# Optimization experiments

Measured on AMD Instinct MI355X. Metric: run time of the kernel, lower is better.

The kernel has to match this reference:

```python
import jax, jax.numpy as jnp
import numpy as np

EPS = 1e-5
N_GRAPHS = 64


def gcn_conv(x, W, b, src, dst, n_nodes):
    # GCNConv: out = D^{-1/2} (A + I) D^{-1/2} X W + b
    xw = x @ W  # [N, H]
    # add self loops
    loops = jnp.arange(n_nodes, dtype=src.dtype)
    src_f = jnp.concatenate([src, loops])
    dst_f = jnp.concatenate([dst, loops])
    deg = jax.ops.segment_sum(jnp.ones_like(dst_f, dtype=xw.dtype), dst_f, num_segments=n_nodes)
    dinv = jnp.where(deg > 0, jax.lax.rsqrt(deg), 0.0)
    norm = dinv[src_f] * dinv[dst_f]  # [E+N]
    msg = xw[src_f] * norm[:, None]  # gather + scale
    out = jax.ops.segment_sum(msg, dst_f, num_segments=n_nodes)  # scatter-add
    return out + b


def batchnorm(x):
    # fresh BatchNorm1d in training mode: identity affine, batch stats, biased var
    mean = jnp.mean(x, axis=0)
    var = jnp.mean((x - mean) ** 2, axis=0)
    return (x - mean) * jax.lax.rsqrt(var + EPS)


def setup_inputs() -> dict:
    key = jax.random.key(0)
    ks = jax.random.split(key, 12)
    N, E, F, H, C = 65536, 1048576, 64, 64, 16
    x = jax.random.normal(ks[0], (N, F), dtype=jnp.float32)
    edge_index = jax.random.randint(ks[1], (2, E), 0, N, dtype=jnp.int64)
    batch = jnp.sort(jax.random.randint(ks[2], (N,), 0, N_GRAPHS, dtype=jnp.int64))
    s = 1.0 / np.sqrt(H)
    W0 = jax.random.normal(ks[3], (F, H), dtype=jnp.float32) * s
    b0 = jax.random.normal(ks[4], (H,), dtype=jnp.float32) * 0.1
    W1 = jax.random.normal(ks[5], (H, H), dtype=jnp.float32) * s
    b1 = jax.random.normal(ks[6], (H,), dtype=jnp.float32) * 0.1
    W2 = jax.random.normal(ks[7], (H, H), dtype=jnp.float32) * s
    b2 = jax.random.normal(ks[8], (H,), dtype=jnp.float32) * 0.1
    clf_W = jax.random.normal(ks[9], (C, H), dtype=jnp.float32) * s
    clf_b = jax.random.normal(ks[10], (C,), dtype=jnp.float32) * 0.1
    return {"x": x, "edge_index": edge_index, "batch": batch,
            "W0": W0, "b0": b0, "W1": W1, "b1": b1, "W2": W2, "b2": b2,
            "clf_W": clf_W, "clf_b": clf_b}


def reference(x, edge_index, batch, W0, b0, W1, b1, W2, b2, clf_W, clf_b):
    n_nodes = x.shape[0]
    src, dst = edge_index[0], edge_index[1]
    weights = [(W0, b0), (W1, b1), (W2, b2)]
    n_conv = len(weights)
    h = x
    for i, (W, b) in enumerate(weights):
        h = gcn_conv(h, W, b, src, dst, n_nodes)
        if i < n_conv - 1:
            h = jax.nn.relu(h)
        h = batchnorm(h)
    # global mean pool over graphs
    sums = jax.ops.segment_sum(h, batch, num_segments=N_GRAPHS)
    cnts = jax.ops.segment_sum(jnp.ones((n_nodes,), h.dtype), batch, num_segments=N_GRAPHS)
    pooled = sums / jnp.maximum(cnts, 1.0)[:, None]
    logits = pooled @ clf_W.T + clf_b
    return jax.nn.softmax(logits, axis=1)
```

## Files before the change

### kernel.cpp

```cpp
#include <hip/hip_runtime.h>
#include <hip/hip_fp16.h>


#define NBKT 512
#define CAP  4096
#define BSTRIDE 16

__device__ inline unsigned pack2h(float a, float b) {
    __half ha = __float2half_rn(a), hb = __float2half_rn(b);
    unsigned short ua = *(unsigned short*)&ha, ub = *(unsigned short*)&hb;
    return (unsigned)ua | ((unsigned)ub << 16);
}

__device__ inline void acc8(float* a, uint4 u) {
    __half2* hp = (__half2*)&u;
#pragma unroll
    for (int i = 0; i < 4; ++i) {
        float2 f = __half22float2(hp[i]);
        a[2 * i] += f.x;
        a[2 * i + 1] += f.y;
    }
}

__global__ void k_binit(int* __restrict__ bcur) {
    int t = blockIdx.x * 256 + threadIdx.x;
    if (t < NBKT) bcur[t * BSTRIDE] = t * CAP;
}

__global__ void k_bin(const int* __restrict__ ei, int E, int* __restrict__ bcur,
                      int* __restrict__ buck) {
    __shared__ int sd[4096];
    __shared__ unsigned short bk[4096];
    __shared__ int cnt[NBKT], off[NBKT];
    int t = threadIdx.x;
    int base = blockIdx.x * 4096;
    for (int i = t; i < NBKT; i += 256) cnt[i] = 0;
    __syncthreads();
#pragma unroll
    for (int k = 0; k < 16; ++k) {
        int i = k * 256 + t;
        int e = base + i;
        int s = ei[e], d = ei[E + e];
        sd[i] = (s << 7) | (d & 127);
        int b = d >> 7;
        bk[i] = (unsigned short)b;
        atomicAdd(&cnt[b], 1);
    }
    __syncthreads();
    for (int b = t; b < NBKT; b += 256) {
        int c = cnt[b];
        off[b] = c ? atomicAdd(&bcur[b * BSTRIDE], c) : 0;
    }
    __syncthreads();
#pragma unroll
    for (int k = 0; k < 16; ++k) {
        int i = k * 256 + t;
        int b = bk[i];
        int p = atomicAdd(&off[b], 1);
        buck[p] = sd[i];
    }
}

__global__ void k_scanB(const int* __restrict__ bcur, int* __restrict__ bbase,
                        int* __restrict__ rowptr, float* __restrict__ psum,
                        float* __restrict__ pcnt, int N, int E) {
    __shared__ int s[NBKT];
    int t = threadIdx.x;
    int v = bcur[t * BSTRIDE] - t * CAP;
    s[t] = v;
    __syncthreads();
    for (int o = 1; o < NBKT; o <<= 1) {
        int x = (t >= o) ? s[t - o] : 0;
        __syncthreads();
        s[t] += x;
        __syncthreads();
    }
    bbase[t] = s[t] - v;
    for (int i = t; i < 4096; i += NBKT) psum[i] = 0.0f;
    if (t < 64) pcnt[t] = 0.0f;
    if (t == 0) rowptr[N] = E;
}

__global__ void k_place(const int* __restrict__ bcur, const int* __restrict__ buck,
                        const int* __restrict__ bbase, int* __restrict__ rowptr,
                        float* __restrict__ dinv, int* __restrict__ csr) {
    __shared__ int dc[128], sc[128], cur[128];
    int b = blockIdx.x, t = threadIdx.x;
    if (t < 128) dc[t] = 0;
    __syncthreads();
    int beg = b * CAP, end = bcur[b * BSTRIDE];
    for (int i = beg + t; i < end; i += 256) atomicAdd(&dc[buck[i] & 127], 1);
    __syncthreads();
    int v = (t < 128) ? dc[t] : 0;
    if (t < 128) sc[t] = v;
    __syncthreads();
    for (int o = 1; o < 128; o <<= 1) {
        int x = 0;
        if (t < 128 && t >= o) x = sc[t - o];
        __syncthreads();
        if (t < 128) sc[t] += x;
        __syncthreads();
    }
    if (t < 128) {
        int r = bbase[b] + sc[t] - v;
        rowptr[b * 128 + t] = r;
        cur[t] = r;
        dinv[b * 128 + t] = rsqrtf((float)(v + 1));
    }
    __syncthreads();
    for (int i = beg + t; i < end; i += 256) {
        int e = buck[i];
        int p = atomicAdd(&cur[e & 127], 1);
        csr[p] = e >> 7;
    }
}

template <int HIN>
__global__ void k_gemm(const void* __restrict__ hv, const float* __restrict__ W,
                       const float* __restrict__ mean, const float* __restrict__ rstd,
                       int has_stats, const float* __restrict__ dinv,
                       __half* __restrict__ y) {
    __shared__ float Ws[4096];
    __shared__ float hs[64 * 65];
    __shared__ float sm[64], sr[64], bs[64];
    int t = threadIdx.x;
    int rowBase = blockIdx.x * 64;
    if (t < 64) {
        sm[t] = has_stats ? mean[t] : 0.0f;
        sr[t] = has_stats ? rstd[t] : 1.0f;
    }
    __syncthreads();
#pragma unroll
    for (int k = 0; k < 4; ++k) {
        int i = t + k * 256;
        float4 wv = ((const float4*)W)[i];
        float s = sr[i >> 4];
        wv.x *= s; wv.y *= s; wv.z *= s; wv.w *= s;
        ((float4*)Ws)[i] = wv;
    }
    if (HIN) {
        const uint4* src = (const uint4*)((const __half*)hv + (size_t)rowBase * 64);
#pragma unroll
        for (int k = 0; k < 2; ++k) {
            int i = t + k * 256;
            int row = i >> 3, c8 = i & 7;
            uint4 u = src[i];
            const __half2* hp = (const __half2*)&u;
            float* dst = &hs[row * 65 + c8 * 8];
#pragma unroll
            for (int j = 0; j < 4; ++j) {
                dst[2 * j + 0] = __low2float(hp[j]);
                dst[2 * j + 1] = __high2float(hp[j]);
            }
        }
    } else {
        const float4* src = (const float4*)((const float*)hv + (size_t)rowBase * 64);
#pragma unroll
        for (int k = 0; k < 4; ++k) {
            int i = t + k * 256;
            int row = i >> 4, c4 = i & 15;
            float4 v = src[i];
            float* dst = &hs[row * 65 + c4 * 4];
            dst[0] = v.x; dst[1] = v.y; dst[2] = v.z; dst[3] = v.w;
        }
    }
    __syncthreads();
    if (t < 64) {
        float acc = 0.0f;
        for (int f = 0; f < 64; ++f) acc += sm[f] * Ws[f * 64 + t];
        bs[t] = -acc;
    }
    __syncthreads();
    int rg = t >> 4;
    int cg = t & 15;
    float4 a0, a1, a2, a3;
    {
        float bx = bs[cg * 4 + 0], by = bs[cg * 4 + 1];
        float bz = bs[cg * 4 + 2], bw = bs[cg * 4 + 3];
        a0 = {bx, by, bz, bw}; a1 = a0; a2 = a0; a3 = a0;
    }
    const float* h0 = &hs[(rg * 4 + 0) * 65];
    const float* h1 = &hs[(rg * 4 + 1) * 65];
    const float* h2 = &hs[(rg * 4 + 2) * 65];
    const float* h3 = &hs[(rg * 4 + 3) * 65];
#pragma unroll 4
    for (int f = 0; f < 64; ++f) {
        float4 wv = ((float4*)Ws)[f * 16 + cg];
        float v0 = h0[f], v1 = h1[f], v2 = h2[f], v3 = h3[f];
        a0.x += v0 * wv.x; a0.y += v0 * wv.y; a0.z += v0 * wv.z; a0.w += v0 * wv.w;
        a1.x += v1 * wv.x; a1.y += v1 * wv.y; a1.z += v1 * wv.z; a1.w += v1 * wv.w;
        a2.x += v2 * wv.x; a2.y += v2 * wv.y; a2.z += v2 * wv.z; a2.w += v2 * wv.w;
        a3.x += v3 * wv.x; a3.y += v3 * wv.y; a3.z += v3 * wv.z; a3.w += v3 * wv.w;
    }
    float d0 = dinv[rowBase + rg * 4 + 0];
    float d1 = dinv[rowBase + rg * 4 + 1];
    float d2 = dinv[rowBase + rg * 4 + 2];
    float d3 = dinv[rowBase + rg * 4 + 3];
    uint2* y2 = (uint2*)y;
    size_t ob = (size_t)(rowBase + rg * 4) * 16 + cg;
    y2[ob + 0]  = {pack2h(a0.x * d0, a0.y * d0), pack2h(a0.z * d0, a0.w * d0)};
    y2[ob + 16] = {pack2h(a1.x * d1, a1.y * d1), pack2h(a1.z * d1, a1.w * d1)};
    y2[ob + 32] = {pack2h(a2.x * d2, a2.y * d2), pack2h(a2.z * d2, a2.w * d2)};
    y2[ob + 48] = {pack2h(a3.x * d3, a3.y * d3), pack2h(a3.z * d3, a3.w * d3)};
}

template <int RELU>
__global__ __launch_bounds__(512) void k_agg(
        const __half* __restrict__ y, const int* __restrict__ rowptr,
        const int* __restrict__ csr, const float* __restrict__ dinv,
        const float* __restrict__ bias, __half* __restrict__ hout,
        float* __restrict__ partials, int N) {
    __shared__ int lcsr[2048];
    __shared__ int lrp[65];
    __shared__ float SW[16][64];
    int t = threadIdx.x;
    int lane = t & 63, wid = t >> 6;
    int o = lane >> 3, j = lane & 7;
    int nodeBase = blockIdx.x * 64;
    if (t < 65) lrp[t] = rowptr[nodeBase + t];
    __syncthreads();
    int wbase = lrp[0];
    int wlen = lrp[64] - wbase;
    bool fits = (wlen <= 2048);
    if (fits)
        for (int i = t; i < wlen; i += 512) lcsr[i] = csr[wbase + i];
    __syncthreads();

    int n = nodeBase + wid * 8 + o;
    int beg = lrp[wid * 8 + o] - wbase;
    int d = lrp[wid * 8 + o + 1] - wbase - beg;
    const uint4* y4 = (const uint4*)y;
    float a[8] = {0, 0, 0, 0, 0, 0, 0, 0};

    if (fits) {
        const int* cp = lcsr + beg;
        int k = 0;
        for (; k + 4 <= d; k += 4) {
            int s0 = cp[k], s1 = cp[k + 1], s2 = cp[k + 2], s3 = cp[k + 3];
            uint4 u0 = y4[(size_t)s0 * 8 + j];
            uint4 u1 = y4[(size_t)s1 * 8 + j];
            uint4 u2 = y4[(size_t)s2 * 8 + j];
            uint4 u3 = y4[(size_t)s3 * 8 + j];
            acc8(a, u0); acc8(a, u1); acc8(a, u2); acc8(a, u3);
        }
        for (; k < d; ++k) {
            uint4 u0 = y4[(size_t)cp[k] * 8 + j];
            acc8(a, u0);
        }
    } else {
        const int* cp = csr + wbase + beg;
        int k = 0;
        for (; k + 4 <= d; k += 4) {
            int s0 = cp[k], s1 = cp[k + 1], s2 = cp[k + 2], s3 = cp[k + 3];
            uint4 u0 = y4[(size_t)s0 * 8 + j];
            uint4 u1 = y4[(size_t)s1 * 8 + j];
            uint4 u2 = y4[(size_t)s2 * 8 + j];
            uint4 u3 = y4[(size_t)s3 * 8 + j];
            acc8(a, u0); acc8(a, u1); acc8(a, u2); acc8(a, u3);
        }
        for (; k < d; ++k) {
            uint4 u0 = y4[(size_t)cp[k] * 8 + j];
            acc8(a, u0);
        }
    }
    uint4 us = y4[(size_t)n * 8 + j];
    acc8(a, us);

    float dv = dinv[n];
    const float4* b4 = (const float4*)bias;
    float4 blo = b4[j * 2], bhi = b4[j * 2 + 1];
    float v[8];
    v[0] = a[0] * dv + blo.x; v[1] = a[1] * dv + blo.y;
    v[2] = a[2] * dv + blo.z; v[3] = a[3] * dv + blo.w;
    v[4] = a[4] * dv + bhi.x; v[5] = a[5] * dv + bhi.y;
    v[6] = a[6] * dv + bhi.z; v[7] = a[7] * dv + bhi.w;
    if (RELU) {
#pragma unroll
        for (int i = 0; i < 8; ++i) v[i] = fmaxf(v[i], 0.0f);
    }
    uint4 ov;
    ov.x = pack2h(v[0], v[1]); ov.y = pack2h(v[2], v[3]);
    ov.z = pack2h(v[4], v[5]); ov.w = pack2h(v[6], v[7]);
    ((uint4*)hout)[(size_t)n * 8 + j] = ov;

    float q[8];
#pragma unroll
    for (int i = 0; i < 8; ++i) q[i] = v[i] * v[i];
#pragma unroll
    for (int st = 8; st <= 32; st <<= 1) {
#pragma unroll
        for (int i = 0; i < 8; ++i) {
            v[i] += __shfl_xor(v[i], st);
            q[i] += __shfl_xor(q[i], st);
        }
    }
    if (o == 0) {
#pragma unroll
        for (int i = 0; i < 8; ++i) {
            SW[wid][j * 8 + i] = v[i];
            SW[8 + wid][j * 8 + i] = q[i];
        }
    }
    __syncthreads();
    if (t < 64) {
        float s = 0.0f, qq = 0.0f;
#pragma unroll
        for (int w = 0; w < 8; ++w) {
            s += SW[w][t];
            qq += SW[8 + w][t];
        }
        partials[(size_t)blockIdx.x * 128 + t] = s;
        partials[(size_t)blockIdx.x * 128 + 64 + t] = qq;
    }
}

__global__ void k_stats(const float* __restrict__ partials, int nblk,
                        float* __restrict__ mean, float* __restrict__ rstd, float invN) {
    __shared__ float sh[256];
    int f = blockIdx.x, t = threadIdx.x;
    float s = 0.0f, q = 0.0f;
    for (int b = t; b < nblk; b += 256) {
        s += partials[(size_t)b * 128 + f];
        q += partials[(size_t)b * 128 + 64 + f];
    }
    sh[t] = s;
    __syncthreads();
    for (int o = 128; o > 0; o >>= 1) {
        if (t < o) sh[t] += sh[t + o];
        __syncthreads();
    }
    float S = sh[0];
    __syncthreads();
    sh[t] = q;
    __syncthreads();
    for (int o = 128; o > 0; o >>= 1) {
        if (t < o) sh[t] += sh[t + o];
        __syncthreads();
    }
    if (t == 0) {
        float Qs = sh[0];
        float m = S * invN;
        float var = Qs * invN - m * m;
        mean[f] = m;
        rstd[f] = rsqrtf(var + 1e-5f);
    }
}

__global__ void k_pool(const __half* __restrict__ h, const int* __restrict__ batch,
                       const float* __restrict__ mean, const float* __restrict__ rstd,
                       float* __restrict__ psum, float* __restrict__ pcnt) {
    int lane = threadIdx.x;
    int base = blockIdx.x * 64;
    float m = mean[lane], r = rstd[lane];
    int cur = batch[base];
    float acc = 0.0f;
    int runlen = 0;
    for (int i = 0; i < 64; ++i) {
        int n = base + i;
        int g = batch[n];
        if (g != cur) {
            atomicAdd(&psum[cur * 64 + lane], acc);
            if (lane == 0) atomicAdd(&pcnt[cur], (float)runlen);
            acc = 0.0f;
            runlen = 0;
            cur = g;
        }
        acc += (__half2float(h[(size_t)n * 64 + lane]) - m) * r;
        runlen++;
    }
    atomicAdd(&psum[cur * 64 + lane], acc);
    if (lane == 0) atomicAdd(&pcnt[cur], (float)runlen);
}

__global__ void k_head(const float* __restrict__ psum, const float* __restrict__ pcnt,
                       const float* __restrict__ clfW, const float* __restrict__ clfb,
                       float* __restrict__ out) {
    __shared__ float ps[64 * 64];
    __shared__ float wl[16 * 64];
    __shared__ float ci[64];
    int t = threadIdx.x;
    ((float4*)ps)[t] = ((const float4*)psum)[t];
    if (t < 256) ((float4*)wl)[t] = ((const float4*)clfW)[t];
    if (t < 64) ci[t] = 1.0f / fmaxf(pcnt[t], 1.0f);
    __syncthreads();
    int g = t >> 4, c = t & 15;
    float acc = 0.0f;
#pragma unroll 8
    for (int f = 0; f < 64; ++f) acc += ps[g * 64 + f] * wl[c * 64 + f];
    acc = acc * ci[g] + clfb[c];
    float mx = acc;
    for (int o = 1; o < 16; o <<= 1) mx = fmaxf(mx, __shfl_xor(mx, o, 16));
    float e = __expf(acc - mx);
    float s = e;
    for (int o = 1; o < 16; o <<= 1) s += __shfl_xor(s, o, 16);
    out[t] = e / s;
}

extern "C" void kernel_launch(void* const* d_in, const int* in_sizes, int n_in,
                              void* d_out, int out_size, void* d_ws, size_t ws_size,
                              hipStream_t stream) {
    const float* x    = (const float*)d_in[0];
    const int*   ei   = (const int*)d_in[1];
    const int*   bat  = (const int*)d_in[2];
    const float* W0   = (const float*)d_in[3];
    const float* b0   = (const float*)d_in[4];
    const float* W1   = (const float*)d_in[5];
    const float* b1   = (const float*)d_in[6];
    const float* W2   = (const float*)d_in[7];
    const float* b2   = (const float*)d_in[8];
    const float* clfW = (const float*)d_in[9];
    const float* clfb = (const float*)d_in[10];
    float* out = (float*)d_out;

    const int N = in_sizes[0] / 64;
    const int E = in_sizes[1] / 2;
    const int AB = N / 64;

    char* w = (char*)d_ws;
    size_t off = 0;
    auto take = [&](size_t bytes) -> void* {
        off = (off + 255) & ~(size_t)255;
        void* p = w + off;
        off += bytes;
        return p;
    };
    int*    rowptr   = (int*)take((size_t)(N + 1) * 4);
    int*    bcur     = (int*)take((size_t)NBKT * BSTRIDE * 4);
    int*    bbase    = (int*)take((size_t)NBKT * 4);
    float*  dinv     = (float*)take((size_t)N * 4);
    int*    csr      = (int*)take((size_t)E * 4);
    __half* y        = (__half*)take((size_t)N * 64 * 2);
    __half* hA       = (__half*)take((size_t)N * 64 * 2);
    __half* hB       = (__half*)take((size_t)N * 64 * 2);
    float*  partials = (float*)take((size_t)AB * 128 * 4);
    float*  mean     = (float*)take(256);
    float*  rstd     = (float*)take(256);
    float*  psum     = (float*)take(64 * 64 * 4);
    float*  pcnt     = (float*)take(64 * 4);
    int* buck = (int*)hB;

    k_binit<<<(NBKT + 255) / 256, 256, 0, stream>>>(bcur);
    k_bin<<<E / 4096, 256, 0, stream>>>(ei, E, bcur, buck);
    k_scanB<<<1, NBKT, 0, stream>>>(bcur, bbase, rowptr, psum, pcnt, N, E);
    k_place<<<NBKT, 256, 0, stream>>>(bcur, buck, bbase, rowptr, dinv, csr);

    const float invN = 1.0f / (float)N;

    k_gemm<0><<<N / 64, 256, 0, stream>>>(x, W0, mean, rstd, 0, dinv, y);
    k_agg<1><<<AB, 512, 0, stream>>>(y, rowptr, csr, dinv, b0, hA, partials, N);
    k_stats<<<64, 256, 0, stream>>>(partials, AB, mean, rstd, invN);

    k_gemm<1><<<N / 64, 256, 0, stream>>>(hA, W1, mean, rstd, 1, dinv, y);
    k_agg<1><<<AB, 512, 0, stream>>>(y, rowptr, csr, dinv, b1, hB, partials, N);
    k_stats<<<64, 256, 0, stream>>>(partials, AB, mean, rstd, invN);

    k_gemm<1><<<N / 64, 256, 0, stream>>>(hB, W2, mean, rstd, 1, dinv, y);
    k_agg<0><<<AB, 512, 0, stream>>>(y, rowptr, csr, dinv, b2, hA, partials, N);
    k_stats<<<64, 256, 0, stream>>>(partials, AB, mean, rstd, invN);

    k_pool<<<N / 64, 64, 0, stream>>>(hA, bat, mean, rstd, psum, pcnt);
    k_head<<<1, 1024, 0, stream>>>(psum, pcnt, clfW, clfb, out);
}
```

Baseline: 188.4 us.

## Fold BN stats into agg via atomics, drop k_stats, vectorize GEMM, enlarge binning tiles

Removes the three k_stats reduction kernels. Each aggregation block now atomically adds its per-feature sum and sum-of-squares into padded global accumulators, and the next GEMM or the pool kernel derives mean and rstd inline. The GEMM inner loop is changed to float4 LDS reads with a 68-float row stride, and the binning kernel handles 8192 edges per block instead of 4096. This cuts three launches and a pass over the partials array, at the cost of float atomic contention (1024 blocks per address) and nondeterministic summation order.

```diff
diff --git a/kernel.cpp b/kernel.cpp
--- a/kernel.cpp
+++ b/kernel.cpp
@@ -22,6 +22,10 @@
     }
 }
 
+__device__ inline void fma4(float4& acc, float s, float4 w) {
+    acc.x += s * w.x; acc.y += s * w.y; acc.z += s * w.z; acc.w += s * w.w;
+}
+
 __global__ void k_binit(int* __restrict__ bcur) {
     int t = blockIdx.x * 256 + threadIdx.x;
     if (t < NBKT) bcur[t * BSTRIDE] = t * CAP;
@@ -29,15 +33,15 @@
 
 __global__ void k_bin(const int* __restrict__ ei, int E, int* __restrict__ bcur,
                       int* __restrict__ buck) {
-    __shared__ int sd[4096];
-    __shared__ unsigned short bk[4096];
+    __shared__ int sd[8192];
+    __shared__ unsigned short bk[8192];
     __shared__ int cnt[NBKT], off[NBKT];
     int t = threadIdx.x;
-    int base = blockIdx.x * 4096;
+    int base = blockIdx.x * 8192;
     for (int i = t; i < NBKT; i += 256) cnt[i] = 0;
     __syncthreads();
 #pragma unroll
-    for (int k = 0; k < 16; ++k) {
+    for (int k = 0; k < 32; ++k) {
         int i = k * 256 + t;
         int e = base + i;
         int s = ei[e], d = ei[E + e];
@@ -53,7 +57,7 @@
     }
     __syncthreads();
 #pragma unroll
-    for (int k = 0; k < 16; ++k) {
+    for (int k = 0; k < 32; ++k) {
         int i = k * 256 + t;
         int b = bk[i];
         int p = atomicAdd(&off[b], 1);
@@ -62,8 +66,9 @@
 }
 
 __global__ void k_scanB(const int* __restrict__ bcur, int* __restrict__ bbase,
-                        int* __restrict__ rowptr, float* __restrict__ psum,
-                        float* __restrict__ pcnt, int N, int E) {
+                        int* __restrict__ rowptr, float* __restrict__ gstats,
+                        float* __restrict__ psum, float* __restrict__ pcnt,
+                        int N, int E) {
     __shared__ int s[NBKT];
     int t = threadIdx.x;
     int v = bcur[t * BSTRIDE] - t * CAP;
@@ -76,6 +81,7 @@
         __syncthreads();
     }
     bbase[t] = s[t] - v;
+    for (int i = t; i < 3 * 2048; i += NBKT) gstats[i] = 0.0f;
     for (int i = t; i < 4096; i += NBKT) psum[i] = 0.0f;
     if (t < 64) pcnt[t] = 0.0f;
     if (t == 0) rowptr[N] = E;
@@ -115,19 +121,27 @@
     }
 }
 
-template <int HIN>
+template <int HIN, int HS>
 __global__ void k_gemm(const void* __restrict__ hv, const float* __restrict__ W,
-                       const float* __restrict__ mean, const float* __restrict__ rstd,
-                       int has_stats, const float* __restrict__ dinv,
-                       __half* __restrict__ y) {
+                       const float* __restrict__ gstats, float invN,
+                       const float* __restrict__ dinv, __half* __restrict__ y) {
     __shared__ float Ws[4096];
-    __shared__ float hs[64 * 65];
+    __shared__ float hs[64 * 68];
     __shared__ float sm[64], sr[64], bs[64];
     int t = threadIdx.x;
     int rowBase = blockIdx.x * 64;
     if (t < 64) {
-        sm[t] = has_stats ? mean[t] : 0.0f;
-        sr[t] = has_stats ? rstd[t] : 1.0f;
+        if (HS) {
+            float S = gstats[t * 16];
+            float Q = gstats[(64 + t) * 16];
+            float m = S * invN;
+            float var = Q * invN - m * m;
+            sm[t] = m;
+            sr[t] = rsqrtf(var + 1e-5f);
+        } else {
+            sm[t] = 0.0f;
+            sr[t] = 1.0f;
+        }
     }
     __syncthreads();
 #pragma unroll
@@ -146,7 +160,7 @@
             int row = i >> 3, c8 = i & 7;
             uint4 u = src[i];
             const __half2* hp = (const __half2*)&u;
-            float* dst = &hs[row * 65 + c8 * 8];
+            float* dst = &hs[row * 68 + c8 * 8];
 #pragma unroll
             for (int j = 0; j < 4; ++j) {
                 dst[2 * j + 0] = __low2float(hp[j]);
@@ -160,8 +174,7 @@
             int i = t + k * 256;
             int row = i >> 4, c4 = i & 15;
             float4 v = src[i];
-            float* dst = &hs[row * 65 + c4 * 4];
-            dst[0] = v.x; dst[1] = v.y; dst[2] = v.z; dst[3] = v.w;
+            *(float4*)&hs[row * 68 + c4 * 4] = v;
         }
     }
     __syncthreads();
@@ -179,18 +192,22 @@
         float bz = bs[cg * 4 + 2], bw = bs[cg * 4 + 3];
         a0 = {bx, by, bz, bw}; a1 = a0; a2 = a0; a3 = a0;
     }
-    const float* h0 = &hs[(rg * 4 + 0) * 65];
-    const float* h1 = &hs[(rg * 4 + 1) * 65];
-    const float* h2 = &hs[(rg * 4 + 2) * 65];
-    const float* h3 = &hs[(rg * 4 + 3) * 65];
+    const float4* Ws4 = (const float4*)Ws;
+    const float4* H0 = (const float4*)&hs[(rg * 4 + 0) * 68];
+    const float4* H1 = (const float4*)&hs[(rg * 4 + 1) * 68];
+    const float4* H2 = (const float4*)&hs[(rg * 4 + 2) * 68];
+    const float4* H3 = (const float4*)&hs[(rg * 4 + 3) * 68];
 #pragma unroll 4
-    for (int f = 0; f < 64; ++f) {
-        float4 wv = ((float4*)Ws)[f * 16 + cg];
-        float v0 = h0[f], v1 = h1[f], v2 = h2[f], v3 = h3[f];
-        a0.x += v0 * wv.x; a0.y += v0 * wv.y; a0.z += v0 * wv.z; a0.w += v0 * wv.w;
-        a1.x += v1 * wv.x; a1.y += v1 * wv.y; a1.z += v1 * wv.z; a1.w += v1 * wv.w;
-        a2.x += v2 * wv.x; a2.y += v2 * wv.y; a2.z += v2 * wv.z; a2.w += v2 * wv.w;
-        a3.x += v3 * wv.x; a3.y += v3 * wv.y; a3.z += v3 * wv.z; a3.w += v3 * wv.w;
+    for (int f4 = 0; f4 < 16; ++f4) {
+        float4 w0 = Ws4[(4 * f4 + 0) * 16 + cg];
+        float4 w1 = Ws4[(4 * f4 + 1) * 16 + cg];
+        float4 w2 = Ws4[(4 * f4 + 2) * 16 + cg];
+        float4 w3 = Ws4[(4 * f4 + 3) * 16 + cg];
+        float4 h0v = H0[f4], h1v = H1[f4], h2v = H2[f4], h3v = H3[f4];
+        fma4(a0, h0v.x, w0); fma4(a0, h0v.y, w1); fma4(a0, h0v.z, w2); fma4(a0, h0v.w, w3);
+        fma4(a1, h1v.x, w0); fma4(a1, h1v.y, w1); fma4(a1, h1v.z, w2); fma4(a1, h1v.w, w3);
+        fma4(a2, h2v.x, w0); fma4(a2, h2v.y, w1); fma4(a2, h2v.z, w2); fma4(a2, h2v.w, w3);
+        fma4(a3, h3v.x, w0); fma4(a3, h3v.y, w1); fma4(a3, h3v.z, w2); fma4(a3, h3v.w, w3);
     }
     float d0 = dinv[rowBase + rg * 4 + 0];
     float d1 = dinv[rowBase + rg * 4 + 1];
@@ -209,7 +226,7 @@
         const __half* __restrict__ y, const int* __restrict__ rowptr,
         const int* __restrict__ csr, const float* __restrict__ dinv,
         const float* __restrict__ bias, __half* __restrict__ hout,
-        float* __restrict__ partials, int N) {
+        float* __restrict__ gstats, int N) {
     __shared__ int lcsr[2048];
     __shared__ int lrp[65];
     __shared__ float SW[16][64];
@@ -309,49 +326,19 @@
             s += SW[w][t];
             qq += SW[8 + w][t];
         }
-        partials[(size_t)blockIdx.x * 128 + t] = s;
-        partials[(size_t)blockIdx.x * 128 + 64 + t] = qq;
-    }
-}
-
-__global__ void k_stats(const float* __restrict__ partials, int nblk,
-                        float* __restrict__ mean, float* __restrict__ rstd, float invN) {
-    __shared__ float sh[256];
-    int f = blockIdx.x, t = threadIdx.x;
-    float s = 0.0f, q = 0.0f;
-    for (int b = t; b < nblk; b += 256) {
-        s += partials[(size_t)b * 128 + f];
-        q += partials[(size_t)b * 128 + 64 + f];
-    }
-    sh[t] = s;
-    __syncthreads();
-    for (int o = 128; o > 0; o >>= 1) {
-        if (t < o) sh[t] += sh[t + o];
-        __syncthreads();
-    }
-    float S = sh[0];
-    __syncthreads();
-    sh[t] = q;
-    __syncthreads();
-    for (int o = 128; o > 0; o >>= 1) {
-        if (t < o) sh[t] += sh[t + o];
-        __syncthreads();
-    }
-    if (t == 0) {
-        float Qs = sh[0];
-        float m = S * invN;
-        float var = Qs * invN - m * m;
-        mean[f] = m;
-        rstd[f] = rsqrtf(var + 1e-5f);
+        atomicAdd(&gstats[t * 16], s);
+        atomicAdd(&gstats[(64 + t) * 16], qq);
     }
 }
 
 __global__ void k_pool(const __half* __restrict__ h, const int* __restrict__ batch,
-                       const float* __restrict__ mean, const float* __restrict__ rstd,
+                       const float* __restrict__ gstats, float invN,
                        float* __restrict__ psum, float* __restrict__ pcnt) {
     int lane = threadIdx.x;
     int base = blockIdx.x * 64;
-    float m = mean[lane], r = rstd[lane];
+    float S = gstats[lane * 16], Q = gstats[(64 + lane) * 16];
+    float m = S * invN;
+    float r = rsqrtf(Q * invN - m * m + 1e-5f);
     int cur = batch[base];
     float acc = 0.0f;
     int runlen = 0;
@@ -432,32 +419,28 @@
     __half* y        = (__half*)take((size_t)N * 64 * 2);
     __half* hA       = (__half*)take((size_t)N * 64 * 2);
     __half* hB       = (__half*)take((size_t)N * 64 * 2);
-    float*  partials = (float*)take((size_t)AB * 128 * 4);
-    float*  mean     = (float*)take(256);
-    float*  rstd     = (float*)take(256);
+    float*  gstats   = (float*)take((size_t)3 * 2048 * 4);
     float*  psum     = (float*)take(64 * 64 * 4);
     float*  pcnt     = (float*)take(64 * 4);
     int* buck = (int*)hB;
+    float* gs0 = gstats;
+    float* gs1 = gstats + 2048;
+    float* gs2 = gstats + 4096;
+
+    const float invN = 1.0f / (float)N;
 
     k_binit<<<(NBKT + 255) / 256, 256, 0, stream>>>(bcur);
-    k_bin<<<E / 4096, 256, 0, stream>>>(ei, E, bcur, buck);
-    k_scanB<<<1, NBKT, 0, stream>>>(bcur, bbase, rowptr, psum, pcnt, N, E);
+    k_bin<<<E / 8192, 256, 0, stream>>>(ei, E, bcur, buck);
+    k_scanB<<<1, NBKT, 0, stream>>>(bcur, bbase, rowptr, gstats, psum, pcnt, N, E);
     k_place<<<NBKT, 256, 0, stream>>>(bcur, buck, bbase, rowptr, dinv, csr);
 
-    const float invN = 1.0f / (float)N;
-
-    k_gemm<0><<<N / 64, 256, 0, stream>>>(x, W0, mean, rstd, 0, dinv, y);
-    k_agg<1><<<AB, 512, 0, stream>>>(y, rowptr, csr, dinv, b0, hA, partials, N);
-    k_stats<<<64, 256, 0, stream>>>(partials, AB, mean, rstd, invN);
-
-    k_gemm<1><<<N / 64, 256, 0, stream>>>(hA, W1, mean, rstd, 1, dinv, y);
-    k_agg<1><<<AB, 512, 0, stream>>>(y, rowptr, csr, dinv, b1, hB, partials, N);
-    k_stats<<<64, 256, 0, stream>>>(partials, AB, mean, rstd, invN);
-
-    k_gemm<1><<<N / 64, 256, 0, stream>>>(hB, W2, mean, rstd, 1, dinv, y);
-    k_agg<0><<<AB, 512, 0, stream>>>(y, rowptr, csr, dinv, b2, hA, partials, N);
-    k_stats<<<64, 256, 0, stream>>>(partials, AB, mean, rstd, invN);
-
-    k_pool<<<N / 64, 64, 0, stream>>>(hA, bat, mean, rstd, psum, pcnt);
+    k_gemm<0, 0><<<N / 64, 256, 0, stream>>>(x, W0, nullptr, invN, dinv, y);
+    k_agg<1><<<AB, 512, 0, stream>>>(y, rowptr, csr, dinv, b0, hA, gs0, N);
+    k_gemm<1, 1><<<N / 64, 256, 0, stream>>>(hA, W1, gs0, invN, dinv, y);
+    k_agg<1><<<AB, 512, 0, stream>>>(y, rowptr, csr, dinv, b1, hB, gs1, N);
+    k_gemm<1, 1><<<N / 64, 256, 0, stream>>>(hB, W2, gs1, invN, dinv, y);
+    k_agg<0><<<AB, 512, 0, stream>>>(y, rowptr, csr, dinv, b2, hA, gs2, N);
+
+    k_pool<<<N / 64, 64, 0, stream>>>(hA, bat, gs2, invN, psum, pcnt);
     k_head<<<1, 1024, 0, stream>>>(psum, pcnt, clfW, clfb, out);
 }
```

Result: slower. 231.0 us (+22.6%).
